# Performance work log

Measured on AMD Instinct MI355X. Metric: run time of the kernel, lower is better.

Reference implementation:

```python
import jax, jax.numpy as jnp
import numpy as np

ALPHA = 0.5
REG_RATIO = 0.5


def _xavier(key, shape):
    fan_in, fan_out = shape
    lim = np.sqrt(6.0 / (fan_in + fan_out))
    return jax.random.uniform(key, shape, minval=-lim, maxval=lim, dtype=jnp.float32)


def setup_inputs() -> dict:
    key = jax.random.key(0)
    ks = jax.random.split(key, 5)
    B, T, I, H, O = 128, 512, 4, 512, 3
    return {
        "x": jax.random.normal(ks[0], (B, T, I), dtype=jnp.float32),
        "h": jax.random.normal(ks[1], (B, H), dtype=jnp.float32),
        "W_rec": _xavier(ks[2], (H, H)),
        "W_in": _xavier(ks[3], (I, H)),
        "W_out": _xavier(ks[4], (H, O)),
        "bias_rec": jnp.zeros((H,), dtype=jnp.float32),
        "bias_in": jnp.zeros((H,), dtype=jnp.float32),
    }


def reference(x, h, W_rec, W_in, W_out, bias_rec, bias_in):
    # x: (B, T, I), h: (B, H)
    B, T, _ = x.shape
    H = h.shape[1]
    n_reg = round(H * REG_RATIO)
    alpha = jnp.asarray(ALPHA, x.dtype)
    # add_noise=False -> noise term is zero
    xt = jnp.swapaxes(x, 0, 1)                     # (T, B, I)
    flags = (jnp.arange(T) > 0).astype(x.dtype)    # z_old reg term skipped at t=0

    def step(carry, inp):
        h_prev, z_prev, reg = carry
        x_t, flag = inp
        # z = W_rec-recurrence + input drive (h_rec + h_in in the torch code)
        z_new = jnp.tanh(h_prev) @ W_rec + bias_rec + x_t @ W_in + bias_in  # (B, H)
        h_new = (1.0 - alpha) * h_prev + alpha * z_new
        # note: h_from_prev / (1 - alpha) == h_prev
        reg = (reg
               + jnp.sum((h_new[:, :n_reg] - h_prev[:, :n_reg]) ** 2)
               + flag * jnp.sum((z_new[:, :n_reg] - z_prev[:, :n_reg]) ** 2))
        out = h_new @ W_out                        # (B, O)
        return (h_new, z_new, reg), (h_new, out)

    init = (h, jnp.zeros_like(h), jnp.asarray(0.0, x.dtype))
    (_, _, reg), (hs, outs) = jax.lax.scan(step, init, (xt, flags))

    hidden_states = jnp.concatenate([h[None], hs], axis=0)  # (T+1, B, H)
    outputs = jnp.swapaxes(outs, 0, 1)                      # (B, T, O)
    tcr_reg = reg / T / B / n_reg
    return outputs, hidden_states, tcr_reg
```

## Files before the change

kernel.cpp:

```cpp
#include <hip/hip_runtime.h>
#include <math.h>


#define BB 128
#define TT 512
#define II 4
#define HH 512
#define OO 3
#define NREG_ 256

#define NTHREADS 512
#define MEMBERS 4
#define ROWS 2
#define NGROUPS 64
#define NBLOCKS (NGROUPS * MEMBERS)

#define WS_ADAT  0
#define WS_PART  (2 * NGROUPS * 2 * HH * 8)

typedef unsigned long long u64;
typedef unsigned int u32;
typedef __attribute__((ext_vector_type(2))) float f32x2;

__device__ __forceinline__ u64 aload(const u64* p) {
    return __hip_atomic_load(p, __ATOMIC_RELAXED, __HIP_MEMORY_SCOPE_AGENT);
}
__device__ __forceinline__ void astore(u64* p, u64 v) {
    __hip_atomic_store(p, v, __ATOMIC_RELAXED, __HIP_MEMORY_SCOPE_AGENT);
}
__device__ __forceinline__ float rlane(float v, int l) {
    return __uint_as_float(__builtin_amdgcn_readlane(__float_as_uint(v), l));
}
__device__ __forceinline__ float fast_tanh(float x) {
    float ax = fabsf(x);
    float e  = __expf(2.0f * ax);
    float r  = 1.0f - 2.0f * __builtin_amdgcn_rcpf(e + 1.0f);
    return copysignf(r, x);
}

#define R16(M) M(0) M(1) M(2) M(3) M(4) M(5) M(6) M(7) \
               M(8) M(9) M(10) M(11) M(12) M(13) M(14) M(15)

#define WLD(Q) \
    f32x2 w##Q##a, w##Q##b, w##Q##c, w##Q##d; \
    w##Q##a.x = Wp[(size_t)(4*Q+0)*HH]; w##Q##a.y = Wp[(size_t)(4*Q+0)*HH+64]; \
    w##Q##b.x = Wp[(size_t)(4*Q+1)*HH]; w##Q##b.y = Wp[(size_t)(4*Q+1)*HH+64]; \
    w##Q##c.x = Wp[(size_t)(4*Q+2)*HH]; w##Q##c.y = Wp[(size_t)(4*Q+2)*HH+64]; \
    w##Q##d.x = Wp[(size_t)(4*Q+3)*HH]; w##Q##d.y = Wp[(size_t)(4*Q+3)*HH+64];

#define KSTEP(K, W) { \
    float s0 = rlane(ar0, (K)); \
    float s1 = rlane(ar1, (K)); \
    accA.x = fmaf(s0, W.x, accA.x); \
    accA.y = fmaf(s1, W.x, accA.y); \
    accB.x = fmaf(s0, W.y, accB.x); \
    accB.y = fmaf(s1, W.y, accB.y); }

#define MV(Q) KSTEP(4*Q+0, w##Q##a) KSTEP(4*Q+1, w##Q##b) \
              KSTEP(4*Q+2, w##Q##c) KSTEP(4*Q+3, w##Q##d)

__global__ __launch_bounds__(NTHREADS) __attribute__((amdgpu_waves_per_eu(2, 2)))
void rnn_main(const float* __restrict__ x,
              const float* __restrict__ h0,
              const float* __restrict__ W_rec,
              const float* __restrict__ W_in,
              const float* __restrict__ bias_rec,
              const float* __restrict__ bias_in,
              float* __restrict__ hidden,
              u64* __restrict__ adat,
              float* __restrict__ partials)
{
    const int tid  = threadIdx.x;
    const int bid  = blockIdx.x;
    const int xcd  = bid & 7;
    const int onx  = bid >> 3;
    const int memb = onx & (MEMBERS - 1);
    const int g    = xcd * 8 + (onx >> 2);
    const int r0   = g * ROWS;
    const int wid  = tid >> 6;
    const int lane = tid & 63;

    __shared__ float sc_s[2][ROWS][128][9];
    __shared__ float xbuf[ROWS * TT * II];
    __shared__ float win_s[II][128];
    __shared__ float ub_s[128];
    __shared__ float red_s[NTHREADS / 64];

    for (int idx = tid; idx < ROWS * TT * II; idx += NTHREADS) {
        int r = idx >> 11, rem = idx & (TT * II - 1);
        xbuf[idx] = x[(size_t)(r0 + r) * (TT * II) + rem];
    }
    if (tid < II * 128) {
        int i = tid >> 7, jj = tid & 127;
        win_s[i][jj] = W_in[i * HH + memb * 128 + jj];
    }
    if (tid < 128) {
        ub_s[tid] = bias_rec[memb * 128 + tid] + bias_in[memb * 128 + tid];
    }

    const float* Wp = W_rec + (size_t)(wid * 64) * HH + memb * 128 + lane;
    R16(WLD)

    const int fr  = tid >> 7;
    const int fj  = tid & 127;
    const int fjg = memb * 128 + fj;
    float hprev = 0.0f, zprev = 0.0f, racc = 0.0f;
    if (tid < ROWS * 128) {
        hprev = h0[(size_t)(r0 + fr) * HH + fjg];
        u64 pv = (u64)__float_as_uint(hprev) | ((u64)1u << 32);
        astore(&adat[((size_t)(0 * NGROUPS + g) * 2 + fr) * HH + fjg], pv);
        hidden[(size_t)(r0 + fr) * HH + fjg] = hprev;
    }

#pragma unroll 1
    for (int t = 0; t < TT; ++t) {
        const int slot = t & 1;
        const u32 tagc = (u32)(t + 1);

        const u64* p0 = adat + ((size_t)(slot * NGROUPS + g) * 2) * HH
                        + wid * 64 + lane;
        const u64* p1 = p0 + HH;
        u64 u0, u1;
        for (;;) {
            u0 = aload(p0);
            u1 = aload(p1);
            bool ok = ((u32)(u0 >> 32) == tagc) & ((u32)(u1 >> 32) == tagc);
            if (__all(ok)) break;
        }
        float ar0 = fast_tanh(__uint_as_float((u32)u0));
        float ar1 = fast_tanh(__uint_as_float((u32)u1));

        f32x2 accA = {0.0f, 0.0f};
        f32x2 accB = {0.0f, 0.0f};
        R16(MV)

        sc_s[slot][0][lane][wid]      = accA.x;
        sc_s[slot][1][lane][wid]      = accA.y;
        sc_s[slot][0][lane + 64][wid] = accB.x;
        sc_s[slot][1][lane + 64][wid] = accB.y;
        __syncthreads();

        if (tid < ROWS * 128) {
            float q0 = sc_s[slot][fr][fj][0], q1 = sc_s[slot][fr][fj][1];
            float q2 = sc_s[slot][fr][fj][2], q3 = sc_s[slot][fr][fj][3];
            float q4 = sc_s[slot][fr][fj][4], q5 = sc_s[slot][fr][fj][5];
            float q6 = sc_s[slot][fr][fj][6], q7 = sc_s[slot][fr][fj][7];
            float z = ((q0 + q1) + (q2 + q3)) + ((q4 + q5) + (q6 + q7));
            z += ub_s[fj];
            const float* xr = &xbuf[fr * (TT * II) + t * II];
            z = fmaf(xr[0], win_s[0][fj], z);
            z = fmaf(xr[1], win_s[1][fj], z);
            z = fmaf(xr[2], win_s[2][fj], z);
            z = fmaf(xr[3], win_s[3][fj], z);
            float hn = 0.5f * hprev + 0.5f * z;
            const int slot2 = (t + 1) & 1;
            u64 pv = (u64)__float_as_uint(hn) | ((u64)(tagc + 1) << 32);
            astore(&adat[((size_t)(slot2 * NGROUPS + g) * 2 + fr) * HH + fjg], pv);
            hidden[(size_t)(t + 1) * BB * HH + (size_t)(r0 + fr) * HH + fjg] = hn;
            if (fjg < NREG_) {
                float d1 = hn - hprev;
                racc = fmaf(d1, d1, racc);
                if (t > 0) { float d2 = z - zprev; racc = fmaf(d2, d2, racc); }
                zprev = z;
            }
            hprev = hn;
        }
    }

    for (int off = 32; off; off >>= 1) racc += __shfl_down(racc, off);
    if ((tid & 63) == 0) red_s[tid >> 6] = racc;
    __syncthreads();
    if (tid == 0) {
        float s = 0.0f;
        for (int i = 0; i < NTHREADS / 64; ++i) s += red_s[i];
        partials[g * MEMBERS + memb] = s;
    }
}

__global__ __launch_bounds__(256)
void rnn_out(const float* __restrict__ hidden,
             const float* __restrict__ W_out,
             float* __restrict__ outputs)
{
    __shared__ float wout_s[HH * OO];
    const int tid = threadIdx.x;
    for (int i = tid; i < HH * OO; i += 256) wout_s[i] = W_out[i];
    __syncthreads();

    const int gid  = blockIdx.x * 4 + (tid >> 6);
    const int lane = tid & 63;
    const int b = gid >> 9;
    const int t = gid & (TT - 1);
    const float* hp = hidden + (size_t)(t + 1) * BB * HH + (size_t)b * HH;

    float o0 = 0.0f, o1 = 0.0f, o2 = 0.0f;
#pragma unroll
    for (int q = 0; q < 8; ++q) {
        int k = lane + 64 * q;
        float hv = hp[k];
        o0 = fmaf(hv, wout_s[k * 3 + 0], o0);
        o1 = fmaf(hv, wout_s[k * 3 + 1], o1);
        o2 = fmaf(hv, wout_s[k * 3 + 2], o2);
    }
    for (int off = 32; off; off >>= 1) {
        o0 += __shfl_down(o0, off);
        o1 += __shfl_down(o1, off);
        o2 += __shfl_down(o2, off);
    }
    if (lane == 0) {
        float* op = outputs + (size_t)(b * TT + t) * OO;
        op[0] = o0; op[1] = o1; op[2] = o2;
    }
}

__global__ __launch_bounds__(256)
void rnn_tcr(const float* __restrict__ partials, float* __restrict__ tcr)
{
    __shared__ float red[4];
    const int tid = threadIdx.x;
    float v = partials[tid];
    for (int off = 32; off; off >>= 1) v += __shfl_down(v, off);
    if ((tid & 63) == 0) red[tid >> 6] = v;
    __syncthreads();
    if (tid == 0) {
        float s = red[0] + red[1] + red[2] + red[3];
        *tcr = s * (1.0f / ((float)TT * (float)BB * (float)NREG_));
    }
}

extern "C" void kernel_launch(void* const* d_in, const int* in_sizes, int n_in,
                              void* d_out, int out_size, void* d_ws, size_t ws_size,
                              hipStream_t stream)
{
    (void)in_sizes; (void)n_in; (void)out_size; (void)ws_size;

    const float* x     = (const float*)d_in[0];
    const float* h0    = (const float*)d_in[1];
    const float* W_rec = (const float*)d_in[2];
    const float* W_in  = (const float*)d_in[3];
    const float* W_out = (const float*)d_in[4];
    const float* brec  = (const float*)d_in[5];
    const float* bin   = (const float*)d_in[6];

    float* out     = (float*)d_out;
    float* outputs = out;
    float* hidden  = out + (size_t)BB * TT * OO;
    float* tcr     = out + (size_t)BB * TT * OO + (size_t)(TT + 1) * BB * HH;

    u64*   adat     = (u64*)((char*)d_ws + WS_ADAT);
    float* partials = (float*)((char*)d_ws + WS_PART);

    (void)hipMemsetAsync(d_ws, 0, WS_PART, stream);

    void* args[] = { (void*)&x, (void*)&h0, (void*)&W_rec, (void*)&W_in,
                     (void*)&brec, (void*)&bin, (void*)&hidden,
                     (void*)&adat, (void*)&partials };
    (void)hipLaunchCooperativeKernel((const void*)rnn_main,
                                     dim3(NBLOCKS), dim3(NTHREADS),
                                     args, 0, stream);

    rnn_out<<<dim3((BB * TT) / 4), dim3(256), 0, stream>>>(hidden, W_out, outputs);
    rnn_tcr<<<dim3(1), dim3(256), 0, stream>>>(partials, tcr);
}
```

Before: 1.206 ms.

## Split each group's two batch rows into staggered half-steps with packed FMA

Each block group now handles two independent batch rows, g and 64+g, as two separate recurrence chains. Within a timestep the block processes row A and then row B, each with its own flag-wait, matvec and reduce, so the exchange latency of one chain can overlap with compute on the other. The tanh is moved to the producer, which publishes tanh(h) instead of h, so consumers skip recomputing it. The inner loop uses inline v_pk_fma_f32 with one scalar broadcast per k instead of two readlanes. The cost is two barriers and two global waits per step instead of one.

```diff
diff --git a/kernel.cpp b/kernel.cpp
--- a/kernel.cpp
+++ b/kernel.cpp
@@ -11,12 +11,10 @@
 
 #define NTHREADS 512
 #define MEMBERS 4
-#define ROWS 2
 #define NGROUPS 64
 #define NBLOCKS (NGROUPS * MEMBERS)
 
-#define WS_ADAT  0
-#define WS_PART  (2 * NGROUPS * 2 * HH * 8)
+#define WS_PART  (2 * 2 * NGROUPS * HH * 8)
 
 typedef unsigned long long u64;
 typedef unsigned int u32;
@@ -27,9 +25,6 @@
 }
 __device__ __forceinline__ void astore(u64* p, u64 v) {
     __hip_atomic_store(p, v, __ATOMIC_RELAXED, __HIP_MEMORY_SCOPE_AGENT);
-}
-__device__ __forceinline__ float rlane(float v, int l) {
-    return __uint_as_float(__builtin_amdgcn_readlane(__float_as_uint(v), l));
 }
 __device__ __forceinline__ float fast_tanh(float x) {
     float ax = fabsf(x);
@@ -49,12 +44,10 @@
     w##Q##d.x = Wp[(size_t)(4*Q+3)*HH]; w##Q##d.y = Wp[(size_t)(4*Q+3)*HH+64];
 
 #define KSTEP(K, W) { \
-    float s0 = rlane(ar0, (K)); \
-    float s1 = rlane(ar1, (K)); \
-    accA.x = fmaf(s0, W.x, accA.x); \
-    accA.y = fmaf(s1, W.x, accA.y); \
-    accB.x = fmaf(s0, W.y, accB.x); \
-    accB.y = fmaf(s1, W.y, accB.y); }
+    u32 s_ = __builtin_amdgcn_readlane(__float_as_uint(ar), (K)); \
+    u64 ss = (u64)s_; \
+    asm("v_pk_fma_f32 %0, %1, %2, %0 op_sel_hi:[0,1,1]" \
+        : "+v"(acc) : "s"(ss), "v"(W)); }
 
 #define MV(Q) KSTEP(4*Q+0, w##Q##a) KSTEP(4*Q+1, w##Q##b) \
               KSTEP(4*Q+2, w##Q##c) KSTEP(4*Q+3, w##Q##d)
@@ -76,19 +69,20 @@
     const int onx  = bid >> 3;
     const int memb = onx & (MEMBERS - 1);
     const int g    = xcd * 8 + (onx >> 2);
-    const int r0   = g * ROWS;
+    const int rA   = g;
+    const int rB   = 64 + g;
     const int wid  = tid >> 6;
     const int lane = tid & 63;
 
-    __shared__ float sc_s[2][ROWS][128][9];
-    __shared__ float xbuf[ROWS * TT * II];
+    __shared__ float sc_s[2][128][9];
+    __shared__ float xbuf[2][TT * II];
     __shared__ float win_s[II][128];
     __shared__ float ub_s[128];
     __shared__ float red_s[NTHREADS / 64];
 
-    for (int idx = tid; idx < ROWS * TT * II; idx += NTHREADS) {
-        int r = idx >> 11, rem = idx & (TT * II - 1);
-        xbuf[idx] = x[(size_t)(r0 + r) * (TT * II) + rem];
+    for (int idx = tid; idx < TT * II; idx += NTHREADS) {
+        xbuf[0][idx] = x[(size_t)rA * (TT * II) + idx];
+        xbuf[1][idx] = x[(size_t)rB * (TT * II) + idx];
     }
     if (tid < II * 128) {
         int i = tid >> 7, jj = tid & 127;
@@ -101,69 +95,109 @@
     const float* Wp = W_rec + (size_t)(wid * 64) * HH + memb * 128 + lane;
     R16(WLD)
 
-    const int fr  = tid >> 7;
     const int fj  = tid & 127;
     const int fjg = memb * 128 + fj;
-    float hprev = 0.0f, zprev = 0.0f, racc = 0.0f;
-    if (tid < ROWS * 128) {
-        hprev = h0[(size_t)(r0 + fr) * HH + fjg];
-        u64 pv = (u64)__float_as_uint(hprev) | ((u64)1u << 32);
-        astore(&adat[((size_t)(0 * NGROUPS + g) * 2 + fr) * HH + fjg], pv);
-        hidden[(size_t)(r0 + fr) * HH + fjg] = hprev;
+    float hprevA = 0.0f, zprevA = 0.0f;
+    float hprevB = 0.0f, zprevB = 0.0f;
+    float racc = 0.0f;
+    if (tid < 128) {
+        hprevA = h0[(size_t)rA * HH + fjg];
+        hprevB = h0[(size_t)rB * HH + fjg];
+        u64 pA = (u64)__float_as_uint(fast_tanh(hprevA)) | ((u64)1u << 32);
+        u64 pB = (u64)__float_as_uint(fast_tanh(hprevB)) | ((u64)1u << 32);
+        astore(&adat[((size_t)(0 * 2 + 0) * NGROUPS + g) * HH + fjg], pA);
+        astore(&adat[((size_t)(1 * 2 + 0) * NGROUPS + g) * HH + fjg], pB);
+        hidden[(size_t)rA * HH + fjg] = hprevA;
+        hidden[(size_t)rB * HH + fjg] = hprevB;
     }
 
 #pragma unroll 1
     for (int t = 0; t < TT; ++t) {
-        const int slot = t & 1;
-        const u32 tagc = (u32)(t + 1);
-
-        const u64* p0 = adat + ((size_t)(slot * NGROUPS + g) * 2) * HH
-                        + wid * 64 + lane;
-        const u64* p1 = p0 + HH;
-        u64 u0, u1;
-        for (;;) {
-            u0 = aload(p0);
-            u1 = aload(p1);
-            bool ok = ((u32)(u0 >> 32) == tagc) & ((u32)(u1 >> 32) == tagc);
-            if (__all(ok)) break;
-        }
-        float ar0 = fast_tanh(__uint_as_float((u32)u0));
-        float ar1 = fast_tanh(__uint_as_float((u32)u1));
-
-        f32x2 accA = {0.0f, 0.0f};
-        f32x2 accB = {0.0f, 0.0f};
-        R16(MV)
-
-        sc_s[slot][0][lane][wid]      = accA.x;
-        sc_s[slot][1][lane][wid]      = accA.y;
-        sc_s[slot][0][lane + 64][wid] = accB.x;
-        sc_s[slot][1][lane + 64][wid] = accB.y;
+        const int slot  = t & 1;
+        const int slot2 = (t + 1) & 1;
+        const u32 tagc  = (u32)(t + 1);
+        const u64 tagp  = ((u64)(t + 2) << 32);
+
+        {
+            const u64* pp = adat + ((size_t)(0 * 2 + slot) * NGROUPS + g) * HH
+                            + wid * 64 + lane;
+            u64 u;
+            for (;;) {
+                u = aload(pp);
+                if (__all((u32)(u >> 32) == tagc)) break;
+            }
+            float ar = __uint_as_float((u32)u);
+
+            f32x2 acc = {0.0f, 0.0f};
+            R16(MV)
+            sc_s[0][lane][wid]      = acc.x;
+            sc_s[0][lane + 64][wid] = acc.y;
+        }
         __syncthreads();
-
-        if (tid < ROWS * 128) {
-            float q0 = sc_s[slot][fr][fj][0], q1 = sc_s[slot][fr][fj][1];
-            float q2 = sc_s[slot][fr][fj][2], q3 = sc_s[slot][fr][fj][3];
-            float q4 = sc_s[slot][fr][fj][4], q5 = sc_s[slot][fr][fj][5];
-            float q6 = sc_s[slot][fr][fj][6], q7 = sc_s[slot][fr][fj][7];
+        if (tid < 128) {
+            float q0 = sc_s[0][fj][0], q1 = sc_s[0][fj][1];
+            float q2 = sc_s[0][fj][2], q3 = sc_s[0][fj][3];
+            float q4 = sc_s[0][fj][4], q5 = sc_s[0][fj][5];
+            float q6 = sc_s[0][fj][6], q7 = sc_s[0][fj][7];
             float z = ((q0 + q1) + (q2 + q3)) + ((q4 + q5) + (q6 + q7));
             z += ub_s[fj];
-            const float* xr = &xbuf[fr * (TT * II) + t * II];
+            const float* xr = &xbuf[0][t * II];
             z = fmaf(xr[0], win_s[0][fj], z);
             z = fmaf(xr[1], win_s[1][fj], z);
             z = fmaf(xr[2], win_s[2][fj], z);
             z = fmaf(xr[3], win_s[3][fj], z);
-            float hn = 0.5f * hprev + 0.5f * z;
-            const int slot2 = (t + 1) & 1;
-            u64 pv = (u64)__float_as_uint(hn) | ((u64)(tagc + 1) << 32);
-            astore(&adat[((size_t)(slot2 * NGROUPS + g) * 2 + fr) * HH + fjg], pv);
-            hidden[(size_t)(t + 1) * BB * HH + (size_t)(r0 + fr) * HH + fjg] = hn;
+            float hn = 0.5f * hprevA + 0.5f * z;
+            u64 pv = (u64)__float_as_uint(fast_tanh(hn)) | tagp;
+            astore(&adat[((size_t)(0 * 2 + slot2) * NGROUPS + g) * HH + fjg], pv);
+            hidden[(size_t)(t + 1) * BB * HH + (size_t)rA * HH + fjg] = hn;
             if (fjg < NREG_) {
-                float d1 = hn - hprev;
+                float d1 = hn - hprevA;
                 racc = fmaf(d1, d1, racc);
-                if (t > 0) { float d2 = z - zprev; racc = fmaf(d2, d2, racc); }
-                zprev = z;
-            }
-            hprev = hn;
+                if (t > 0) { float d2 = z - zprevA; racc = fmaf(d2, d2, racc); }
+                zprevA = z;
+            }
+            hprevA = hn;
+        }
+
+        {
+            const u64* pp = adat + ((size_t)(1 * 2 + slot) * NGROUPS + g) * HH
+                            + wid * 64 + lane;
+            u64 u;
+            for (;;) {
+                u = aload(pp);
+                if (__all((u32)(u >> 32) == tagc)) break;
+            }
+            float ar = __uint_as_float((u32)u);
+
+            f32x2 acc = {0.0f, 0.0f};
+            R16(MV)
+            sc_s[1][lane][wid]      = acc.x;
+            sc_s[1][lane + 64][wid] = acc.y;
+        }
+        __syncthreads();
+        if (tid < 128) {
+            float q0 = sc_s[1][fj][0], q1 = sc_s[1][fj][1];
+            float q2 = sc_s[1][fj][2], q3 = sc_s[1][fj][3];
+            float q4 = sc_s[1][fj][4], q5 = sc_s[1][fj][5];
+            float q6 = sc_s[1][fj][6], q7 = sc_s[1][fj][7];
+            float z = ((q0 + q1) + (q2 + q3)) + ((q4 + q5) + (q6 + q7));
+            z += ub_s[fj];
+            const float* xr = &xbuf[1][t * II];
+            z = fmaf(xr[0], win_s[0][fj], z);
+            z = fmaf(xr[1], win_s[1][fj], z);
+            z = fmaf(xr[2], win_s[2][fj], z);
+            z = fmaf(xr[3], win_s[3][fj], z);
+            float hn = 0.5f * hprevB + 0.5f * z;
+            u64 pv = (u64)__float_as_uint(fast_tanh(hn)) | tagp;
+            astore(&adat[((size_t)(1 * 2 + slot2) * NGROUPS + g) * HH + fjg], pv);
+            hidden[(size_t)(t + 1) * BB * HH + (size_t)rB * HH + fjg] = hn;
+            if (fjg < NREG_) {
+                float d1 = hn - hprevB;
+                racc = fmaf(d1, d1, racc);
+                if (t > 0) { float d2 = z - zprevB; racc = fmaf(d2, d2, racc); }
+                zprevB = z;
+            }
+            hprevB = hn;
         }
     }
 
@@ -247,7 +281,7 @@
     float* hidden  = out + (size_t)BB * TT * OO;
     float* tcr     = out + (size_t)BB * TT * OO + (size_t)(TT + 1) * BB * HH;
 
-    u64*   adat     = (u64*)((char*)d_ws + WS_ADAT);
+    u64*   adat     = (u64*)d_ws;
     float* partials = (float*)((char*)d_ws + WS_PART);
 
     (void)hipMemsetAsync(d_ws, 0, WS_PART, stream);
```

Result: faster. 987.1 us (-18.1%).
